# Kernel optimization log

Hardware: AMD Instinct MI355X
Metric: run time of the kernel (lower is better)

Reference implementation:

```python
import jax, jax.numpy as jnp
import numpy as np

D = 16       # data dimension
M = 64       # hidden width
ALPHA0 = 1.0 # alpha[0]
H_RES = 1.0  # ResNet step h = 1/(n_layers-1), n_layers=2


def _antideriv_tanh(x):
    # log(exp(x)+exp(-x)), numerically stable
    return jnp.abs(x) + jnp.log1p(jnp.exp(-2.0 * jnp.abs(x)))


def _dtanh(x):
    t = jnp.tanh(x)
    return 1.0 - t * t


def grad_and_hessian_trace(s, w, A, b, K0, b0, K1, b1):
    """OT-Flow analytic grad of Phi and trace of Hessian (w.r.t. first d coords).
    s: (n, d+1) = [x; t]. n_layers=2 -> one residual layer, h=1."""
    d = s.shape[1] - 1
    opening = s @ K0.T + b0                         # (n, m)
    u0 = _antideriv_tanh(opening)                   # (n, m)
    feat1 = u0 @ K1.T + b1                          # (n, m)
    tanhopen = jnp.tanh(opening)                    # (n, m)
    # backward pass for gradient: z1 = w + h K1^T (tanh(feat1) * w)
    z1 = w + H_RES * (jnp.tanh(feat1) * w) @ K1     # (n, m)
    z0 = (tanhopen * z1) @ K0                       # (n, d+1)
    symA = A.T @ A                                  # (d+1, d+1)
    grad = z0 + s @ symA + b                        # (n, d+1)
    # Hessian trace: opening-layer term
    Kopen = K0[:, :d]                               # (m, d)
    trH = (_dtanh(opening) * z1) @ jnp.sum(Kopen**2, axis=1)   # (n,)
    # forward-propagated Jacobian of u0 w.r.t. x: (n, m, d)
    Jac = tanhopen[:, :, None] * Kopen[None, :, :]
    KJ = jnp.einsum('ij,njd->nid', K1, Jac)         # (n, m, d)
    t1 = jnp.einsum('nm,nmd->n', _dtanh(feat1) * w, KJ**2)
    trH = trH + H_RES * t1 + jnp.sum(A[:, :d] ** 2)  # + trace(symA[:d,:d])
    return grad, trH


def odefun(z, t, w, A, b, K0, b0, K1, b1):
    n = z.shape[0]
    x = z[:, :D]
    s = jnp.concatenate([x, jnp.full((n, 1), t, dtype=z.dtype)], axis=1)
    gradPhi, trH = grad_and_hessian_trace(s, w, A, b, K0, b0, K1, b1)
    dx = -(1.0 / ALPHA0) * gradPhi[:, :D]
    dl = -(1.0 / ALPHA0) * trH[:, None]
    dv = 0.5 * jnp.sum(dx * dx, axis=1, keepdims=True)
    dr = jnp.abs(-gradPhi[:, -1:] + ALPHA0 * dv)
    return jnp.concatenate([dx, dl, dv, dr], axis=1)


def step_rk4(f, z, t0, t1):
    h = t1 - t0
    z0 = z
    K = h * f(z0, t0)
    z = z0 + K / 6.0
    K = h * f(z0 + 0.5 * K, t0 + 0.5 * h)
    z = z + K / 3.0
    K = h * f(z0 + 0.5 * K, t0 + 0.5 * h)
    z = z + K / 3.0
    K = h * f(z0 + K, t0 + h)
    z = z + K / 6.0
    return z


def setup_inputs() -> dict:
    key = jax.random.key(0)
    ks = jax.random.split(key, 8)
    n = 32768
    dp1 = D + 1
    x = jax.random.normal(ks[0], (n, D), dtype=jnp.float32)
    w = jax.random.normal(ks[1], (M,), dtype=jnp.float32) / np.sqrt(M)
    A = 0.1 * jax.random.normal(ks[2], (10, dp1), dtype=jnp.float32)
    b = 0.1 * jax.random.normal(ks[3], (dp1,), dtype=jnp.float32)
    K0 = jax.random.normal(ks[4], (M, dp1), dtype=jnp.float32) / np.sqrt(dp1)
    b0 = 0.1 * jax.random.normal(ks[5], (M,), dtype=jnp.float32)
    K1 = jax.random.normal(ks[6], (M, M), dtype=jnp.float32) / np.sqrt(M)
    b1 = 0.1 * jax.random.normal(ks[7], (M,), dtype=jnp.float32)
    return {"x": x, "w": w, "A": A, "b": b, "K0": K0, "b0": b0,
            "K1": K1, "b1": b1, "nt": 8}


def reference(x, w, A, b, K0, b0, K1, b1, nt):
    f = lambda z, t: odefun(z, t, w, A, b, K0, b0, K1, b1)
    h = 1.0 / nt
    z = jnp.concatenate([x, jnp.zeros((x.shape[0], 3), x.dtype)], axis=1)
    for k in range(nt):  # nt is a static python int
        z = step_rk4(f, z, k * h, (k + 1) * h)
    # unpack: (x_latent, log_det, transport_cost, hjb_violation)
    return z[:, :D], z[:, D], z[:, D + 1], z[:, D + 2]
```

## Files before the change

kernel.cpp:

```cpp
#include <hip/hip_runtime.h>
#include <math.h>

typedef __attribute__((ext_vector_type(8))) short bf16x8;
typedef __attribute__((ext_vector_type(4))) float f32x4;

union B8 { bf16x8 v; unsigned u[4]; };

__device__ __forceinline__ unsigned pk2(float lo, float hi) {
  unsigned r;
  asm("v_cvt_pk_bf16_f32 %0, %1, %2" : "=v"(r) : "v"(lo), "v"(hi));
  return r;
}
__device__ __forceinline__ float rcpf(float x) { return __builtin_amdgcn_rcpf(x); }
__device__ __forceinline__ void ldsfence() { asm volatile("s_waitcnt lgkmcnt(0)" ::: "memory"); }

#define MFMA __builtin_amdgcn_mfma_f32_16x16x32_bf16

__global__ void otflow_prep(const float* __restrict__ K0g,
                            const float* __restrict__ Ag,
                            float* __restrict__ ws) {
  __shared__ float Als[170];
  int tid = threadIdx.x;
  for (int idx = tid; idx < 1024; idx += 256) {
    int m = idx >> 4, d = idx & 15;
    ws[idx] = K0g[m * 17 + d];
  }
  if (tid < 170) Als[tid] = Ag[tid];
  if (tid < 64) {
    float s = 0.f;
    for (int d = 0; d < 16; ++d) { float v = K0g[tid * 17 + d]; s += v * v; }
    ws[1320 + tid] = s;
  }
  __syncthreads();
  for (int idx = tid; idx < 289; idx += 256) {
    int j = idx / 17, k2 = idx % 17;
    float s = 0.f;
#pragma unroll
    for (int r = 0; r < 10; ++r) s += Als[r * 17 + j] * Als[r * 17 + k2];
    ws[1024 + idx] = s;
  }
  __syncthreads();
  if (tid == 0) {
    float s = 0.f;
    for (int r = 0; r < 10; ++r)
      for (int j = 0; j < 16; ++j) { float v = Als[r * 17 + j]; s += v * v; }
    ws[1313] = s;
  }
}

__global__ __launch_bounds__(64, 2) void otflow_main(
    const float* __restrict__ xg, const float* __restrict__ wg,
    const float* __restrict__ bg, const float* __restrict__ K0g,
    const float* __restrict__ b0g, const float* __restrict__ K1g,
    const float* __restrict__ b1g, const int* __restrict__ ntg,
    const float* __restrict__ ws, float* __restrict__ out, int n) {
  __shared__ float buf[16 * 68];
  __shared__ float csh[16 * 68];
  __shared__ float qsh[16 * 68];
  __shared__ float tsh[16 * 20];
  __shared__ float b1s[64], wss[64], k0qs[64], b0s[64], tcs[64];

  const int lane = threadIdx.x;
  const int lr = lane & 15;
  const int lg = lane >> 4;

  b1s[lane] = b1g[lane];
  wss[lane] = wg[lane];
  k0qs[lane] = ws[1320 + lane];
  b0s[lane] = b0g[lane];
  tcs[lane] = K0g[lane * 17 + 16];

  const float sumA2 = ws[1313];

  B8 aK0[4], aK0L[4], aK1[8], aK1T[8], aG[6];
  float kop[16];
#pragma unroll
  for (int mi = 0; mi < 4; ++mi) {
    B8 th, tl;
#pragma unroll
    for (int jj = 0; jj < 4; ++jj) {
      float e0 = K0g[(mi * 16 + lr) * 17 + (lg & 1) * 8 + jj * 2];
      float e1 = K0g[(mi * 16 + lr) * 17 + (lg & 1) * 8 + jj * 2 + 1];
      unsigned hh = pk2(e0, e1);
      th.u[jj] = hh;
      float l0 = e0 - __uint_as_float(hh << 16);
      float l1 = e1 - __uint_as_float(hh & 0xffff0000u);
      tl.u[jj] = pk2(l0, l1);
    }
    aK0[mi] = th; aK0L[mi] = tl;
  }
#pragma unroll
  for (int mi = 0; mi < 4; ++mi)
#pragma unroll
    for (int kb = 0; kb < 2; ++kb) {
      const float* pp = K1g + (mi * 16 + lr) * 64 + kb * 32 + lg * 8;
      float4 q0 = *(const float4*)pp;
      float4 q1 = *(const float4*)(pp + 4);
      B8 t;
      t.u[0] = pk2(q0.x, q0.y); t.u[1] = pk2(q0.z, q0.w);
      t.u[2] = pk2(q1.x, q1.y); t.u[3] = pk2(q1.z, q1.w);
      aK1[mi * 2 + kb] = t;
    }
#pragma unroll
  for (int mi = 0; mi < 4; ++mi)
#pragma unroll
    for (int kb = 0; kb < 2; ++kb) {
      int ib = kb * 32 + lg * 8;
      int m = mi * 16 + lr;
      B8 t;
#pragma unroll
      for (int jj = 0; jj < 4; ++jj)
        t.u[jj] = pk2(K1g[(ib + jj * 2) * 64 + m], K1g[(ib + jj * 2 + 1) * 64 + m]);
      aK1T[mi * 2 + kb] = t;
    }
#pragma unroll
  for (int nb = 0; nb < 2; ++nb)
#pragma unroll
    for (int kb = 0; kb < 3; ++kb) {
      int j = nb * 16 + lr; if (j > 16) j = 16;
      float e[8];
#pragma unroll
      for (int jj = 0; jj < 8; ++jj) {
        float v;
        if (kb < 2) v = K0g[(kb * 32 + lg * 8 + jj) * 17 + j];
        else {
          int kr = lg * 8 + jj;
          v = (kr < 17) ? ws[1024 + kr * 17 + j] : (kr == 17) ? bg[j] : 0.f;
        }
        e[jj] = v;
      }
      B8 t;
      t.u[0] = pk2(e[0], e[1]); t.u[1] = pk2(e[2], e[3]);
      t.u[2] = pk2(e[4], e[5]); t.u[3] = pk2(e[6], e[7]);
      aG[nb * 3 + kb] = t;
    }
#pragma unroll
  for (int kb = 0; kb < 2; ++kb)
#pragma unroll
    for (int j = 0; j < 8; ++j)
      kop[kb * 8 + j] = ws[(kb * 32 + lg * 8 + j) * 16 + lr];

  ldsfence();

  const int nt = *ntg;
  const float h = 1.0f / (float)nt;
  const int p0 = blockIdx.x * 16;
  int pidx = p0 + lr; if (pidx >= n) pidx = n - 1;

  float xin[4], x0s[4], xac[4];
  {
    float4 xi = *(const float4*)(xg + (size_t)pidx * 16 + lg * 4);
    xin[0] = xi.x; xin[1] = xi.y; xin[2] = xi.z; xin[3] = xi.w;
#pragma unroll
    for (int r = 0; r < 4; ++r) { x0s[r] = xin[r]; xac[r] = xin[r]; }
  }
  float lacc = 0.f, vacc = 0.f, racc = 0.f;
  const f32x4 zz = {0.f, 0.f, 0.f, 0.f};

  for (int kstep = 0; kstep < nt; ++kstep) {
    float t0 = (float)kstep * h;
#pragma unroll 1
    for (int st = 0; st < 4; ++st) {
      float tin = t0 + ((st == 0) ? 0.f : (st == 3) ? h : 0.5f * h);

      { float4 xv = {xin[0], xin[1], xin[2], xin[3]};
        *(float4*)(buf + lr * 68 + lg * 4) = xv; }
      ldsfence();
      float4 s0 = *(const float4*)(buf + lr * 68 + (lg & 1) * 8);
      float4 s1 = *(const float4*)(buf + lr * 68 + (lg & 1) * 8 + 4);
      unsigned h0 = pk2(s0.x, s0.y), h1 = pk2(s0.z, s0.w);
      unsigned h2 = pk2(s1.x, s1.y), h3 = pk2(s1.z, s1.w);
      B8 sfO, sfG;
      if (lg < 2) {
        sfO.u[0] = h0; sfO.u[1] = h1; sfO.u[2] = h2; sfO.u[3] = h3;
        sfG.u[0] = h0; sfG.u[1] = h1; sfG.u[2] = h2; sfG.u[3] = h3;
      } else {
        float l0 = s0.x - __uint_as_float(h0 << 16);
        float l1 = s0.y - __uint_as_float(h0 & 0xffff0000u);
        float l2 = s0.z - __uint_as_float(h1 << 16);
        float l3 = s0.w - __uint_as_float(h1 & 0xffff0000u);
        float l4 = s1.x - __uint_as_float(h2 << 16);
        float l5 = s1.y - __uint_as_float(h2 & 0xffff0000u);
        float l6 = s1.z - __uint_as_float(h3 << 16);
        float l7 = s1.w - __uint_as_float(h3 & 0xffff0000u);
        sfO.u[0] = pk2(l0, l1); sfO.u[1] = pk2(l2, l3);
        sfO.u[2] = pk2(l4, l5); sfO.u[3] = pk2(l6, l7);
        if (lg == 2) { sfG.u[0] = pk2(tin, 1.f); sfG.u[1] = 0; sfG.u[2] = 0; sfG.u[3] = 0; }
        else { sfG.u[0] = 0; sfG.u[1] = 0; sfG.u[2] = 0; sfG.u[3] = 0; }
      }

      f32x4 o0 = MFMA(aK0[0].v, sfO.v, zz, 0, 0, 0);
      f32x4 o1 = MFMA(aK0[1].v, sfO.v, zz, 0, 0, 0);
      f32x4 o2 = MFMA(aK0[2].v, sfO.v, zz, 0, 0, 0);
      f32x4 o3 = MFMA(aK0[3].v, sfO.v, zz, 0, 0, 0);
      o0 = MFMA(aK0L[0].v, sfO.v, o0, 0, 0, 0);
      o1 = MFMA(aK0L[1].v, sfO.v, o1, 0, 0, 0);
      o2 = MFMA(aK0L[2].v, sfO.v, o2, 0, 0, 0);
      o3 = MFMA(aK0L[3].v, sfO.v, o3, 0, 0, 0);

      float cva[16];
#pragma unroll
      for (int mi = 0; mi < 4; ++mi) {
        f32x4 oa = (mi == 0) ? o0 : (mi == 1) ? o1 : (mi == 2) ? o2 : o3;
        float4 b0v = *(const float4*)(b0s + mi * 16 + lg * 4);
        float4 tcv = *(const float4*)(tcs + mi * 16 + lg * 4);
        float4 u0v;
#pragma unroll
        for (int r = 0; r < 4; ++r) {
          float ov = oa[r] + fmaf(tin, ((const float*)&tcv)[r], ((const float*)&b0v)[r]);
          float e = __expf(-2.f * fabsf(ov));
          float rp = rcpf(1.f + e);
          float cm = (1.f - e) * rp;
          cva[mi * 4 + r] = __builtin_copysignf(cm, ov);
          ((float*)&u0v)[r] = fabsf(ov) + __logf(1.f + e);
        }
        *(float4*)(buf + lr * 68 + mi * 16 + lg * 4) = u0v;
      }
      ldsfence();

      B8 uf0, uf1;
      {
        const float* bp = buf + lr * 68;
        float4 a0 = *(const float4*)(bp + lg * 8);
        float4 a1 = *(const float4*)(bp + lg * 8 + 4);
        float4 a2 = *(const float4*)(bp + 32 + lg * 8);
        float4 a3 = *(const float4*)(bp + 32 + lg * 8 + 4);
        uf0.u[0] = pk2(a0.x, a0.y); uf0.u[1] = pk2(a0.z, a0.w);
        uf0.u[2] = pk2(a1.x, a1.y); uf0.u[3] = pk2(a1.z, a1.w);
        uf1.u[0] = pk2(a2.x, a2.y); uf1.u[1] = pk2(a2.z, a2.w);
        uf1.u[2] = pk2(a3.x, a3.y); uf1.u[3] = pk2(a3.z, a3.w);
      }
      f32x4 f0 = MFMA(aK1[0].v, uf0.v, zz, 0, 0, 0); f0 = MFMA(aK1[1].v, uf1.v, f0, 0, 0, 0);
      f32x4 f1 = MFMA(aK1[2].v, uf0.v, zz, 0, 0, 0); f1 = MFMA(aK1[3].v, uf1.v, f1, 0, 0, 0);
      f32x4 f2 = MFMA(aK1[4].v, uf0.v, zz, 0, 0, 0); f2 = MFMA(aK1[5].v, uf1.v, f2, 0, 0, 0);
      f32x4 f3 = MFMA(aK1[6].v, uf0.v, zz, 0, 0, 0); f3 = MFMA(aK1[7].v, uf1.v, f3, 0, 0, 0);

#pragma unroll
      for (int mi = 0; mi < 4; ++mi) {
        f32x4 fa = (mi == 0) ? f0 : (mi == 1) ? f1 : (mi == 2) ? f2 : f3;
        float4 b1v = *(const float4*)(b1s + mi * 16 + lg * 4);
        float4 wv = *(const float4*)(wss + mi * 16 + lg * 4);
        float4 av4, qv4;
#pragma unroll
        for (int r = 0; r < 4; ++r) {
          float fv = fa[r] + ((const float*)&b1v)[r];
          float e = __expf(-2.f * fabsf(fv));
          float rp = rcpf(1.f + e);
          float tf = __builtin_copysignf((1.f - e) * rp, fv);
          float wr = ((const float*)&wv)[r];
          ((float*)&av4)[r] = tf * wr;
          ((float*)&qv4)[r] = (1.f - tf * tf) * wr;
        }
        *(float4*)(buf + lr * 68 + mi * 16 + lg * 4) = av4;
        *(float4*)(qsh + lr * 68 + mi * 16 + lg * 4) = qv4;
      }
      ldsfence();

      B8 af0, af1;
      {
        const float* bp = buf + lr * 68;
        float4 a0 = *(const float4*)(bp + lg * 8);
        float4 a1 = *(const float4*)(bp + lg * 8 + 4);
        float4 a2 = *(const float4*)(bp + 32 + lg * 8);
        float4 a3 = *(const float4*)(bp + 32 + lg * 8 + 4);
        af0.u[0] = pk2(a0.x, a0.y); af0.u[1] = pk2(a0.z, a0.w);
        af0.u[2] = pk2(a1.x, a1.y); af0.u[3] = pk2(a1.z, a1.w);
        af1.u[0] = pk2(a2.x, a2.y); af1.u[1] = pk2(a2.z, a2.w);
        af1.u[2] = pk2(a3.x, a3.y); af1.u[3] = pk2(a3.z, a3.w);
      }
      f32x4 z0 = MFMA(aK1T[0].v, af0.v, zz, 0, 0, 0); z0 = MFMA(aK1T[1].v, af1.v, z0, 0, 0, 0);
      f32x4 z1 = MFMA(aK1T[2].v, af0.v, zz, 0, 0, 0); z1 = MFMA(aK1T[3].v, af1.v, z1, 0, 0, 0);
      f32x4 z2 = MFMA(aK1T[4].v, af0.v, zz, 0, 0, 0); z2 = MFMA(aK1T[5].v, af1.v, z2, 0, 0, 0);
      f32x4 z3 = MFMA(aK1T[6].v, af0.v, zz, 0, 0, 0); z3 = MFMA(aK1T[7].v, af1.v, z3, 0, 0, 0);

      float trh_l = 0.f;
#pragma unroll
      for (int mi = 0; mi < 4; ++mi) {
        f32x4 za = (mi == 0) ? z0 : (mi == 1) ? z1 : (mi == 2) ? z2 : z3;
        float4 wv = *(const float4*)(wss + mi * 16 + lg * 4);
        float4 kq = *(const float4*)(k0qs + mi * 16 + lg * 4);
        float4 rv4, cv4;
#pragma unroll
        for (int r = 0; r < 4; ++r) {
          float c = cva[mi * 4 + r];
          float z1v = za[r] + ((const float*)&wv)[r];
          ((float*)&rv4)[r] = c * z1v;
          float dt0 = 1.f - c * c;
          trh_l = fmaf(dt0 * z1v, ((const float*)&kq)[r], trh_l);
          ((float*)&cv4)[r] = c;
        }
        *(float4*)(buf + lr * 68 + mi * 16 + lg * 4) = rv4;
        *(float4*)(csh + lr * 68 + mi * 16 + lg * 4) = cv4;
      }
      trh_l += __shfl_xor(trh_l, 16, 64);
      trh_l += __shfl_xor(trh_l, 32, 64);
      ldsfence();

#pragma unroll 2
      for (int p = 0; p < 16; ++p) {
        const float* cp = csh + p * 68;
        float4 ca = *(const float4*)(cp + lg * 8);
        float4 cb = *(const float4*)(cp + lg * 8 + 4);
        float4 cc = *(const float4*)(cp + 32 + lg * 8);
        float4 cd = *(const float4*)(cp + 32 + lg * 8 + 4);
        B8 y0, y1;
        y0.u[0] = pk2(ca.x * kop[0], ca.y * kop[1]);
        y0.u[1] = pk2(ca.z * kop[2], ca.w * kop[3]);
        y0.u[2] = pk2(cb.x * kop[4], cb.y * kop[5]);
        y0.u[3] = pk2(cb.z * kop[6], cb.w * kop[7]);
        y1.u[0] = pk2(cc.x * kop[8], cc.y * kop[9]);
        y1.u[1] = pk2(cc.z * kop[10], cc.w * kop[11]);
        y1.u[2] = pk2(cd.x * kop[12], cd.y * kop[13]);
        y1.u[3] = pk2(cd.z * kop[14], cd.w * kop[15]);
        f32x4 kc0 = MFMA(y0.v, aK1[0].v, zz, 0, 0, 0); kc0 = MFMA(y1.v, aK1[1].v, kc0, 0, 0, 0);
        f32x4 kc1 = MFMA(y0.v, aK1[2].v, zz, 0, 0, 0); kc1 = MFMA(y1.v, aK1[3].v, kc1, 0, 0, 0);
        f32x4 kc2 = MFMA(y0.v, aK1[4].v, zz, 0, 0, 0); kc2 = MFMA(y1.v, aK1[5].v, kc2, 0, 0, 0);
        f32x4 kc3 = MFMA(y0.v, aK1[6].v, zz, 0, 0, 0); kc3 = MFMA(y1.v, aK1[7].v, kc3, 0, 0, 0);
        float q0 = qsh[p * 68 + lr];
        float q1 = qsh[p * 68 + 16 + lr];
        float q2 = qsh[p * 68 + 32 + lr];
        float q3 = qsh[p * 68 + 48 + lr];
        float d0 = kc0[0] * kc0[0] + kc0[1] * kc0[1] + kc0[2] * kc0[2] + kc0[3] * kc0[3];
        float d1 = kc1[0] * kc1[0] + kc1[1] * kc1[1] + kc1[2] * kc1[2] + kc1[3] * kc1[3];
        float d2 = kc2[0] * kc2[0] + kc2[1] * kc2[1] + kc2[2] * kc2[2] + kc2[3] * kc2[3];
        float d3 = kc3[0] * kc3[0] + kc3[1] * kc3[1] + kc3[2] * kc3[2] + kc3[3] * kc3[3];
        float tp = q0 * d0 + q1 * d1 + q2 * d2 + q3 * d3;
        tp += __shfl_xor(tp, 16, 64);
        tp += __shfl_xor(tp, 32, 64);
        if (lg == 0) tsh[p * 20 + lr] = tp;
      }
      ldsfence();
      float4 tv = *(const float4*)(tsh + lr * 20 + lg * 4);
      float tsum = tv.x + tv.y + tv.z + tv.w;
      tsum += __shfl_xor(tsum, 16, 64);
      tsum += __shfl_xor(tsum, 32, 64);

      B8 rf0, rf1;
      {
        const float* bp = buf + lr * 68;
        float4 a0 = *(const float4*)(bp + lg * 8);
        float4 a1 = *(const float4*)(bp + lg * 8 + 4);
        float4 a2 = *(const float4*)(bp + 32 + lg * 8);
        float4 a3 = *(const float4*)(bp + 32 + lg * 8 + 4);
        rf0.u[0] = pk2(a0.x, a0.y); rf0.u[1] = pk2(a0.z, a0.w);
        rf0.u[2] = pk2(a1.x, a1.y); rf0.u[3] = pk2(a1.z, a1.w);
        rf1.u[0] = pk2(a2.x, a2.y); rf1.u[1] = pk2(a2.z, a2.w);
        rf1.u[2] = pk2(a3.x, a3.y); rf1.u[3] = pk2(a3.z, a3.w);
      }
      f32x4 g0 = MFMA(aG[0].v, rf0.v, zz, 0, 0, 0);
      g0 = MFMA(aG[1].v, rf1.v, g0, 0, 0, 0);
      g0 = MFMA(aG[2].v, sfG.v, g0, 0, 0, 0);
      f32x4 g1 = MFMA(aG[3].v, rf0.v, zz, 0, 0, 0);
      g1 = MFMA(aG[4].v, rf1.v, g1, 0, 0, 0);
      g1 = MFMA(aG[5].v, sfG.v, g1, 0, 0, 0);

      float kx[4];
      float dvp = 0.f;
#pragma unroll
      for (int r = 0; r < 4; ++r) { float d = -g0[r]; kx[r] = d; dvp = fmaf(d, d, dvp); }
      dvp += __shfl_xor(dvp, 16, 64);
      dvp += __shfl_xor(dvp, 32, 64);
      dvp *= 0.5f;
      float g16 = g1[0];
      float trH = trh_l + tsum + sumA2;
      float dl = -trH;
      float dr = fabsf(dvp - g16);
      float wch = ((st == 0 || st == 3) ? (1.f / 6.f) : (1.f / 3.f)) * h;
#pragma unroll
      for (int r = 0; r < 4; ++r) xac[r] = fmaf(wch, kx[r], xac[r]);
      lacc = fmaf(wch, dl, lacc);
      vacc = fmaf(wch, dvp, vacc);
      racc = fmaf(wch, dr, racc);
      if (st < 3) {
        float anh = ((st == 2) ? 1.f : 0.5f) * h;
#pragma unroll
        for (int r = 0; r < 4; ++r) xin[r] = fmaf(anh, kx[r], x0s[r]);
      } else {
#pragma unroll
        for (int r = 0; r < 4; ++r) { x0s[r] = xac[r]; xin[r] = xac[r]; }
      }
    }
  }

  if (p0 + lr < n) {
    float4 xa = {xac[0], xac[1], xac[2], xac[3]};
    *(float4*)(out + (size_t)(p0 + lr) * 16 + lg * 4) = xa;
    if (lg == 0) {
      out[(size_t)n * 16 + p0 + lr] = lacc;
      out[(size_t)n * 17 + p0 + lr] = vacc;
      out[(size_t)n * 18 + p0 + lr] = racc;
    }
  }
}

extern "C" void kernel_launch(void* const* d_in, const int* in_sizes, int n_in,
                              void* d_out, int out_size, void* d_ws, size_t ws_size,
                              hipStream_t stream) {
  const float* xg = (const float*)d_in[0];
  const float* wg = (const float*)d_in[1];
  const float* Ag = (const float*)d_in[2];
  const float* bg = (const float*)d_in[3];
  const float* K0g = (const float*)d_in[4];
  const float* b0g = (const float*)d_in[5];
  const float* K1g = (const float*)d_in[6];
  const float* b1g = (const float*)d_in[7];
  const int* ntg = (const int*)d_in[8];
  float* out = (float*)d_out;
  float* ws = (float*)d_ws;
  int n = in_sizes[0] / 16;

  hipLaunchKernelGGL(otflow_prep, dim3(1), dim3(256), 0, stream, K0g, Ag, ws);
  int nblk = (n + 15) / 16;
  hipLaunchKernelGGL(otflow_main, dim3(nblk), dim3(64), 0, stream,
                     xg, wg, bg, K0g, b0g, K1g, b1g, ntg, ws, out, n);
}
```

Baseline: 358.3 us.

## Split per-block work across two wavefronts with shared-memory exchange

Result: slower. 538.6 us (+50.3%).

```diff
diff --git a/kernel.cpp b/kernel.cpp
--- a/kernel.cpp
+++ b/kernel.cpp
@@ -48,47 +48,55 @@
   }
 }
 
-__global__ __launch_bounds__(64, 2) void otflow_main(
+__global__ __launch_bounds__(128, 2) void otflow_main(
     const float* __restrict__ xg, const float* __restrict__ wg,
     const float* __restrict__ bg, const float* __restrict__ K0g,
     const float* __restrict__ b0g, const float* __restrict__ K1g,
     const float* __restrict__ b1g, const int* __restrict__ ntg,
     const float* __restrict__ ws, float* __restrict__ out, int n) {
-  __shared__ float buf[16 * 68];
+  __shared__ float Xb[16 * 68];
+  __shared__ float Yb[16 * 68];
   __shared__ float csh[16 * 68];
   __shared__ float qsh[16 * 68];
-  __shared__ float tsh[16 * 20];
-  __shared__ float b1s[64], wss[64], k0qs[64], b0s[64], tcs[64];
-
-  const int lane = threadIdx.x;
+  __shared__ float gsh[16 * 20];
+  __shared__ float tsh[16];
+  __shared__ float b0s[64], tcs[64], b1s[64], wss[64], k0qs[64];
+  __shared__ float trhs[32], gsh2[16];
+
+  const int tid = threadIdx.x;
+  const int wid = tid >> 6;
+  const int lane = tid & 63;
   const int lr = lane & 15;
   const int lg = lane >> 4;
 
-  b1s[lane] = b1g[lane];
-  wss[lane] = wg[lane];
-  k0qs[lane] = ws[1320 + lane];
-  b0s[lane] = b0g[lane];
-  tcs[lane] = K0g[lane * 17 + 16];
+  if (wid == 0) {
+    b0s[lane] = b0g[lane];
+    tcs[lane] = K0g[lane * 17 + 16];
+    b1s[lane] = b1g[lane];
+    wss[lane] = wg[lane];
+    k0qs[lane] = ws[1320 + lane];
+  }
 
   const float sumA2 = ws[1313];
 
-  B8 aK0[4], aK0L[4], aK1[8], aK1T[8], aG[6];
-  float kop[16];
-#pragma unroll
-  for (int mi = 0; mi < 4; ++mi) {
+  B8 aK0h[2], aK0l[2];
+#pragma unroll
+  for (int t = 0; t < 2; ++t) {
+    int R = (2 * wid + t) * 16 + lr;
     B8 th, tl;
 #pragma unroll
     for (int jj = 0; jj < 4; ++jj) {
-      float e0 = K0g[(mi * 16 + lr) * 17 + (lg & 1) * 8 + jj * 2];
-      float e1 = K0g[(mi * 16 + lr) * 17 + (lg & 1) * 8 + jj * 2 + 1];
+      float e0 = K0g[R * 17 + (lg & 1) * 8 + jj * 2];
+      float e1 = K0g[R * 17 + (lg & 1) * 8 + jj * 2 + 1];
       unsigned hh = pk2(e0, e1);
       th.u[jj] = hh;
       float l0 = e0 - __uint_as_float(hh << 16);
       float l1 = e1 - __uint_as_float(hh & 0xffff0000u);
       tl.u[jj] = pk2(l0, l1);
     }
-    aK0[mi] = th; aK0L[mi] = tl;
-  }
+    aK0h[t] = th; aK0l[t] = tl;
+  }
+  B8 aK1[8];
 #pragma unroll
   for (int mi = 0; mi < 4; ++mi)
 #pragma unroll
@@ -101,23 +109,24 @@
       t.u[2] = pk2(q1.x, q1.y); t.u[3] = pk2(q1.z, q1.w);
       aK1[mi * 2 + kb] = t;
     }
-#pragma unroll
-  for (int mi = 0; mi < 4; ++mi)
+  B8 aK1T[4];
+#pragma unroll
+  for (int t = 0; t < 2; ++t)
 #pragma unroll
     for (int kb = 0; kb < 2; ++kb) {
       int ib = kb * 32 + lg * 8;
-      int m = mi * 16 + lr;
-      B8 t;
+      int m = (2 * wid + t) * 16 + lr;
+      B8 tt;
 #pragma unroll
       for (int jj = 0; jj < 4; ++jj)
-        t.u[jj] = pk2(K1g[(ib + jj * 2) * 64 + m], K1g[(ib + jj * 2 + 1) * 64 + m]);
-      aK1T[mi * 2 + kb] = t;
-    }
-#pragma unroll
-  for (int nb = 0; nb < 2; ++nb)
+        tt.u[jj] = pk2(K1g[(ib + jj * 2) * 64 + m], K1g[(ib + jj * 2 + 1) * 64 + m]);
+      aK1T[t * 2 + kb] = tt;
+    }
+  B8 aG[3];
+  {
+    int j = wid * 16 + lr; if (j > 16) j = 16;
 #pragma unroll
     for (int kb = 0; kb < 3; ++kb) {
-      int j = nb * 16 + lr; if (j > 16) j = 16;
       float e[8];
 #pragma unroll
       for (int jj = 0; jj < 8; ++jj) {
@@ -132,15 +141,17 @@
       B8 t;
       t.u[0] = pk2(e[0], e[1]); t.u[1] = pk2(e[2], e[3]);
       t.u[2] = pk2(e[4], e[5]); t.u[3] = pk2(e[6], e[7]);
-      aG[nb * 3 + kb] = t;
-    }
+      aG[kb] = t;
+    }
+  }
+  float kop[16];
 #pragma unroll
   for (int kb = 0; kb < 2; ++kb)
 #pragma unroll
     for (int j = 0; j < 8; ++j)
       kop[kb * 8 + j] = ws[(kb * 32 + lg * 8 + j) * 16 + lr];
 
-  ldsfence();
+  __syncthreads();
 
   const int nt = *ntg;
   const float h = 1.0f / (float)nt;
@@ -164,10 +175,10 @@
       float tin = t0 + ((st == 0) ? 0.f : (st == 3) ? h : 0.5f * h);
 
       { float4 xv = {xin[0], xin[1], xin[2], xin[3]};
-        *(float4*)(buf + lr * 68 + lg * 4) = xv; }
+        *(float4*)(Yb + lr * 68 + lg * 4) = xv; }
       ldsfence();
-      float4 s0 = *(const float4*)(buf + lr * 68 + (lg & 1) * 8);
-      float4 s1 = *(const float4*)(buf + lr * 68 + (lg & 1) * 8 + 4);
+      float4 s0 = *(const float4*)(Yb + lr * 68 + (lg & 1) * 8);
+      float4 s1 = *(const float4*)(Yb + lr * 68 + (lg & 1) * 8 + 4);
       unsigned h0 = pk2(s0.x, s0.y), h1 = pk2(s0.z, s0.w);
       unsigned h2 = pk2(s1.x, s1.y), h3 = pk2(s1.z, s1.w);
       B8 sfO, sfG;
@@ -189,38 +200,38 @@
         else { sfG.u[0] = 0; sfG.u[1] = 0; sfG.u[2] = 0; sfG.u[3] = 0; }
       }
 
-      f32x4 o0 = MFMA(aK0[0].v, sfO.v, zz, 0, 0, 0);
-      f32x4 o1 = MFMA(aK0[1].v, sfO.v, zz, 0, 0, 0);
-      f32x4 o2 = MFMA(aK0[2].v, sfO.v, zz, 0, 0, 0);
-      f32x4 o3 = MFMA(aK0[3].v, sfO.v, zz, 0, 0, 0);
-      o0 = MFMA(aK0L[0].v, sfO.v, o0, 0, 0, 0);
-      o1 = MFMA(aK0L[1].v, sfO.v, o1, 0, 0, 0);
-      o2 = MFMA(aK0L[2].v, sfO.v, o2, 0, 0, 0);
-      o3 = MFMA(aK0L[3].v, sfO.v, o3, 0, 0, 0);
-
-      float cva[16];
-#pragma unroll
-      for (int mi = 0; mi < 4; ++mi) {
-        f32x4 oa = (mi == 0) ? o0 : (mi == 1) ? o1 : (mi == 2) ? o2 : o3;
-        float4 b0v = *(const float4*)(b0s + mi * 16 + lg * 4);
-        float4 tcv = *(const float4*)(tcs + mi * 16 + lg * 4);
-        float4 u0v;
+      f32x4 oA[2];
+#pragma unroll
+      for (int t = 0; t < 2; ++t) {
+        oA[t] = MFMA(aK0h[t].v, sfO.v, zz, 0, 0, 0);
+        oA[t] = MFMA(aK0l[t].v, sfO.v, oA[t], 0, 0, 0);
+      }
+      float cva[8];
+#pragma unroll
+      for (int t = 0; t < 2; ++t) {
+        int mrow = (2 * wid + t) * 16;
+        float4 b0v = *(const float4*)(b0s + mrow + lg * 4);
+        float4 tcv = *(const float4*)(tcs + mrow + lg * 4);
+        float4 u0v, cv4;
 #pragma unroll
         for (int r = 0; r < 4; ++r) {
-          float ov = oa[r] + fmaf(tin, ((const float*)&tcv)[r], ((const float*)&b0v)[r]);
+          float ov = oA[t][r] + fmaf(tin, ((const float*)&tcv)[r], ((const float*)&b0v)[r]);
           float e = __expf(-2.f * fabsf(ov));
           float rp = rcpf(1.f + e);
           float cm = (1.f - e) * rp;
-          cva[mi * 4 + r] = __builtin_copysignf(cm, ov);
+          float c = __builtin_copysignf(cm, ov);
+          cva[t * 4 + r] = c;
           ((float*)&u0v)[r] = fabsf(ov) + __logf(1.f + e);
+          ((float*)&cv4)[r] = c;
         }
-        *(float4*)(buf + lr * 68 + mi * 16 + lg * 4) = u0v;
-      }
-      ldsfence();
+        *(float4*)(Xb + lr * 68 + mrow + lg * 4) = u0v;
+        *(float4*)(csh + lr * 68 + mrow + lg * 4) = cv4;
+      }
+      __syncthreads();
 
       B8 uf0, uf1;
       {
-        const float* bp = buf + lr * 68;
+        const float* bp = Xb + lr * 68;
         float4 a0 = *(const float4*)(bp + lg * 8);
         float4 a1 = *(const float4*)(bp + lg * 8 + 4);
         float4 a2 = *(const float4*)(bp + 32 + lg * 8);
@@ -230,20 +241,22 @@
         uf1.u[0] = pk2(a2.x, a2.y); uf1.u[1] = pk2(a2.z, a2.w);
         uf1.u[2] = pk2(a3.x, a3.y); uf1.u[3] = pk2(a3.z, a3.w);
       }
-      f32x4 f0 = MFMA(aK1[0].v, uf0.v, zz, 0, 0, 0); f0 = MFMA(aK1[1].v, uf1.v, f0, 0, 0, 0);
-      f32x4 f1 = MFMA(aK1[2].v, uf0.v, zz, 0, 0, 0); f1 = MFMA(aK1[3].v, uf1.v, f1, 0, 0, 0);
-      f32x4 f2 = MFMA(aK1[4].v, uf0.v, zz, 0, 0, 0); f2 = MFMA(aK1[5].v, uf1.v, f2, 0, 0, 0);
-      f32x4 f3 = MFMA(aK1[6].v, uf0.v, zz, 0, 0, 0); f3 = MFMA(aK1[7].v, uf1.v, f3, 0, 0, 0);
-
-#pragma unroll
-      for (int mi = 0; mi < 4; ++mi) {
-        f32x4 fa = (mi == 0) ? f0 : (mi == 1) ? f1 : (mi == 2) ? f2 : f3;
-        float4 b1v = *(const float4*)(b1s + mi * 16 + lg * 4);
-        float4 wv = *(const float4*)(wss + mi * 16 + lg * 4);
+      f32x4 fA[2];
+#pragma unroll
+      for (int t = 0; t < 2; ++t) {
+        int mi = 2 * wid + t;
+        fA[t] = MFMA(aK1[mi * 2].v, uf0.v, zz, 0, 0, 0);
+        fA[t] = MFMA(aK1[mi * 2 + 1].v, uf1.v, fA[t], 0, 0, 0);
+      }
+#pragma unroll
+      for (int t = 0; t < 2; ++t) {
+        int mrow = (2 * wid + t) * 16;
+        float4 b1v = *(const float4*)(b1s + mrow + lg * 4);
+        float4 wv = *(const float4*)(wss + mrow + lg * 4);
         float4 av4, qv4;
 #pragma unroll
         for (int r = 0; r < 4; ++r) {
-          float fv = fa[r] + ((const float*)&b1v)[r];
+          float fv = fA[t][r] + ((const float*)&b1v)[r];
           float e = __expf(-2.f * fabsf(fv));
           float rp = rcpf(1.f + e);
           float tf = __builtin_copysignf((1.f - e) * rp, fv);
@@ -251,14 +264,14 @@
           ((float*)&av4)[r] = tf * wr;
           ((float*)&qv4)[r] = (1.f - tf * tf) * wr;
         }
-        *(float4*)(buf + lr * 68 + mi * 16 + lg * 4) = av4;
-        *(float4*)(qsh + lr * 68 + mi * 16 + lg * 4) = qv4;
-      }
-      ldsfence();
+        *(float4*)(Yb + lr * 68 + mrow + lg * 4) = av4;
+        *(float4*)(qsh + lr * 68 + mrow + lg * 4) = qv4;
+      }
+      __syncthreads();
 
       B8 af0, af1;
       {
-        const float* bp = buf + lr * 68;
+        const float* bp = Yb + lr * 68;
         float4 a0 = *(const float4*)(bp + lg * 8);
         float4 a1 = *(const float4*)(bp + lg * 8 + 4);
         float4 a2 = *(const float4*)(bp + 32 + lg * 8);
@@ -268,47 +281,47 @@
         af1.u[0] = pk2(a2.x, a2.y); af1.u[1] = pk2(a2.z, a2.w);
         af1.u[2] = pk2(a3.x, a3.y); af1.u[3] = pk2(a3.z, a3.w);
       }
-      f32x4 z0 = MFMA(aK1T[0].v, af0.v, zz, 0, 0, 0); z0 = MFMA(aK1T[1].v, af1.v, z0, 0, 0, 0);
-      f32x4 z1 = MFMA(aK1T[2].v, af0.v, zz, 0, 0, 0); z1 = MFMA(aK1T[3].v, af1.v, z1, 0, 0, 0);
-      f32x4 z2 = MFMA(aK1T[4].v, af0.v, zz, 0, 0, 0); z2 = MFMA(aK1T[5].v, af1.v, z2, 0, 0, 0);
-      f32x4 z3 = MFMA(aK1T[6].v, af0.v, zz, 0, 0, 0); z3 = MFMA(aK1T[7].v, af1.v, z3, 0, 0, 0);
-
+      f32x4 zA[2];
+#pragma unroll
+      for (int t = 0; t < 2; ++t) {
+        zA[t] = MFMA(aK1T[t * 2].v, af0.v, zz, 0, 0, 0);
+        zA[t] = MFMA(aK1T[t * 2 + 1].v, af1.v, zA[t], 0, 0, 0);
+      }
       float trh_l = 0.f;
 #pragma unroll
-      for (int mi = 0; mi < 4; ++mi) {
-        f32x4 za = (mi == 0) ? z0 : (mi == 1) ? z1 : (mi == 2) ? z2 : z3;
-        float4 wv = *(const float4*)(wss + mi * 16 + lg * 4);
-        float4 kq = *(const float4*)(k0qs + mi * 16 + lg * 4);
-        float4 rv4, cv4;
+      for (int t = 0; t < 2; ++t) {
+        int mrow = (2 * wid + t) * 16;
+        float4 wv = *(const float4*)(wss + mrow + lg * 4);
+        float4 kq = *(const float4*)(k0qs + mrow + lg * 4);
+        float4 rv4;
 #pragma unroll
         for (int r = 0; r < 4; ++r) {
-          float c = cva[mi * 4 + r];
-          float z1v = za[r] + ((const float*)&wv)[r];
+          float c = cva[t * 4 + r];
+          float z1v = zA[t][r] + ((const float*)&wv)[r];
           ((float*)&rv4)[r] = c * z1v;
-          float dt0 = 1.f - c * c;
-          trh_l = fmaf(dt0 * z1v, ((const float*)&kq)[r], trh_l);
-          ((float*)&cv4)[r] = c;
+          trh_l = fmaf((1.f - c * c) * z1v, ((const float*)&kq)[r], trh_l);
         }
-        *(float4*)(buf + lr * 68 + mi * 16 + lg * 4) = rv4;
-        *(float4*)(csh + lr * 68 + mi * 16 + lg * 4) = cv4;
+        *(float4*)(Xb + lr * 68 + mrow + lg * 4) = rv4;
       }
       trh_l += __shfl_xor(trh_l, 16, 64);
       trh_l += __shfl_xor(trh_l, 32, 64);
-      ldsfence();
-
-#pragma unroll 2
-      for (int p = 0; p < 16; ++p) {
+      if (lane < 16) trhs[wid * 16 + lane] = trh_l;
+      __syncthreads();
+
+#pragma unroll 1
+      for (int pi = 0; pi < 8; ++pi) {
+        int p = wid * 8 + pi;
         const float* cp = csh + p * 68;
         float4 ca = *(const float4*)(cp + lg * 8);
         float4 cb = *(const float4*)(cp + lg * 8 + 4);
         float4 cc = *(const float4*)(cp + 32 + lg * 8);
         float4 cd = *(const float4*)(cp + 32 + lg * 8 + 4);
         B8 y0, y1;
-        y0.u[0] = pk2(ca.x * kop[0], ca.y * kop[1]);
-        y0.u[1] = pk2(ca.z * kop[2], ca.w * kop[3]);
-        y0.u[2] = pk2(cb.x * kop[4], cb.y * kop[5]);
-        y0.u[3] = pk2(cb.z * kop[6], cb.w * kop[7]);
-        y1.u[0] = pk2(cc.x * kop[8], cc.y * kop[9]);
+        y0.u[0] = pk2(ca.x * kop[0],  ca.y * kop[1]);
+        y0.u[1] = pk2(ca.z * kop[2],  ca.w * kop[3]);
+        y0.u[2] = pk2(cb.x * kop[4],  cb.y * kop[5]);
+        y0.u[3] = pk2(cb.z * kop[6],  cb.w * kop[7]);
+        y1.u[0] = pk2(cc.x * kop[8],  cc.y * kop[9]);
         y1.u[1] = pk2(cc.z * kop[10], cc.w * kop[11]);
         y1.u[2] = pk2(cd.x * kop[12], cd.y * kop[13]);
         y1.u[3] = pk2(cd.z * kop[14], cd.w * kop[15]);
@@ -325,19 +338,14 @@
         float d2 = kc2[0] * kc2[0] + kc2[1] * kc2[1] + kc2[2] * kc2[2] + kc2[3] * kc2[3];
         float d3 = kc3[0] * kc3[0] + kc3[1] * kc3[1] + kc3[2] * kc3[2] + kc3[3] * kc3[3];
         float tp = q0 * d0 + q1 * d1 + q2 * d2 + q3 * d3;
-        tp += __shfl_xor(tp, 16, 64);
-        tp += __shfl_xor(tp, 32, 64);
-        if (lg == 0) tsh[p * 20 + lr] = tp;
-      }
-      ldsfence();
-      float4 tv = *(const float4*)(tsh + lr * 20 + lg * 4);
-      float tsum = tv.x + tv.y + tv.z + tv.w;
-      tsum += __shfl_xor(tsum, 16, 64);
-      tsum += __shfl_xor(tsum, 32, 64);
-
-      B8 rf0, rf1;
+#pragma unroll
+        for (int off = 1; off < 64; off <<= 1) tp += __shfl_xor(tp, off, 64);
+        if (lane == 0) tsh[p] = tp;
+      }
+
       {
-        const float* bp = buf + lr * 68;
+        B8 rf0, rf1;
+        const float* bp = Xb + lr * 68;
         float4 a0 = *(const float4*)(bp + lg * 8);
         float4 a1 = *(const float4*)(bp + lg * 8 + 4);
         float4 a2 = *(const float4*)(bp + 32 + lg * 8);
@@ -346,23 +354,32 @@
         rf0.u[2] = pk2(a1.x, a1.y); rf0.u[3] = pk2(a1.z, a1.w);
         rf1.u[0] = pk2(a2.x, a2.y); rf1.u[1] = pk2(a2.z, a2.w);
         rf1.u[2] = pk2(a3.x, a3.y); rf1.u[3] = pk2(a3.z, a3.w);
-      }
-      f32x4 g0 = MFMA(aG[0].v, rf0.v, zz, 0, 0, 0);
-      g0 = MFMA(aG[1].v, rf1.v, g0, 0, 0, 0);
-      g0 = MFMA(aG[2].v, sfG.v, g0, 0, 0, 0);
-      f32x4 g1 = MFMA(aG[3].v, rf0.v, zz, 0, 0, 0);
-      g1 = MFMA(aG[4].v, rf1.v, g1, 0, 0, 0);
-      g1 = MFMA(aG[5].v, sfG.v, g1, 0, 0, 0);
-
+        f32x4 g = MFMA(aG[0].v, rf0.v, zz, 0, 0, 0);
+        g = MFMA(aG[1].v, rf1.v, g, 0, 0, 0);
+        g = MFMA(aG[2].v, sfG.v, g, 0, 0, 0);
+        if (wid == 0) {
+          float4 gv = {g[0], g[1], g[2], g[3]};
+          *(float4*)(gsh + lr * 20 + lg * 4) = gv;
+        } else if (lane < 16) {
+          gsh2[lane] = g[0];
+        }
+      }
+      __syncthreads();
+
+      float tsum = tsh[lr];
+      float4 gv = *(const float4*)(gsh + lr * 20 + lg * 4);
       float kx[4];
       float dvp = 0.f;
 #pragma unroll
-      for (int r = 0; r < 4; ++r) { float d = -g0[r]; kx[r] = d; dvp = fmaf(d, d, dvp); }
+      for (int r = 0; r < 4; ++r) {
+        float d = -((const float*)&gv)[r];
+        kx[r] = d; dvp = fmaf(d, d, dvp);
+      }
       dvp += __shfl_xor(dvp, 16, 64);
       dvp += __shfl_xor(dvp, 32, 64);
       dvp *= 0.5f;
-      float g16 = g1[0];
-      float trH = trh_l + tsum + sumA2;
+      float g16 = gsh2[lr];
+      float trH = trhs[lr] + trhs[16 + lr] + tsum + sumA2;
       float dl = -trH;
       float dr = fabsf(dvp - g16);
       float wch = ((st == 0 || st == 3) ? (1.f / 6.f) : (1.f / 3.f)) * h;
@@ -383,9 +400,10 @@
   }
 
   if (p0 + lr < n) {
-    float4 xa = {xac[0], xac[1], xac[2], xac[3]};
-    *(float4*)(out + (size_t)(p0 + lr) * 16 + lg * 4) = xa;
-    if (lg == 0) {
+    if (wid == 0) {
+      float4 xa = {xac[0], xac[1], xac[2], xac[3]};
+      *(float4*)(out + (size_t)(p0 + lr) * 16 + lg * 4) = xa;
+    } else if (lg == 0) {
       out[(size_t)n * 16 + p0 + lr] = lacc;
       out[(size_t)n * 17 + p0 + lr] = vacc;
       out[(size_t)n * 18 + p0 + lr] = racc;
@@ -411,6 +429,6 @@
 
   hipLaunchKernelGGL(otflow_prep, dim3(1), dim3(256), 0, stream, K0g, Ag, ws);
   int nblk = (n + 15) / 16;
-  hipLaunchKernelGGL(otflow_main, dim3(nblk), dim3(64), 0, stream,
+  hipLaunchKernelGGL(otflow_main, dim3(nblk), dim3(128), 0, stream,
                      xg, wg, bg, K0g, b0g, K1g, b1g, ntg, ws, out, n);
 }
```
